# Optimization experiments

Measured on AMD Instinct MI355X. Metric: run time of the kernel, lower is better.

Reference implementation:

```python
import jax, jax.numpy as jnp
import numpy as np

EPS = 1e-5
H, W, C, NCLS = 8, 16, 64, 8

def _bn_params(key, c):
    k1, k2, k3, k4 = jax.random.split(key, 4)
    gamma = jax.random.uniform(k1, (c,), minval=0.5, maxval=1.5)
    beta = 0.1 * jax.random.normal(k2, (c,))
    mean = 0.1 * jax.random.normal(k3, (c,))
    var = jax.random.uniform(k4, (c,), minval=0.5, maxval=1.5)
    return jnp.stack([gamma, beta, mean, var]).astype(jnp.float32)  # (4, c)

def bn2d(x, p):
    # eval-mode BatchNorm2d; p: (4, C); x: (B, C, H, W)
    g, b, m, v = p[0], p[1], p[2], p[3]
    s = g * jax.lax.rsqrt(v + EPS)
    return x * s[None, :, None, None] + (b - m * s)[None, :, None, None]

def bn1d_scalar(x, p):
    # eval-mode BatchNorm1d with 1 channel; p: (4, 1); x: (B, 1, F)
    g, b, m, v = p[0], p[1], p[2], p[3]
    s = g * jax.lax.rsqrt(v + EPS)
    return x * s + (b - m * s)

def conv_same(x, w, b):
    y = jax.lax.conv_general_dilated(x, w, (1, 1), 'SAME',
                                     dimension_numbers=('NCHW', 'OIHW', 'NCHW'))
    return y + b[None, :, None, None]

def setup_inputs() -> dict:
    key = jax.random.key(0)
    ks = jax.random.split(key, 24)
    B = 8192
    d = {}
    d['x'] = jax.random.normal(ks[0], (B, 1, H, W), dtype=jnp.float32)
    d['bn0'] = _bn_params(ks[1], 1)
    d['conv1_w'] = 0.1 * jax.random.normal(ks[2], (C, 1, 3, 3), dtype=jnp.float32)
    d['conv1_b'] = jnp.zeros((C,), jnp.float32)
    d['bn1'] = _bn_params(ks[3], C)
    d['conv2_w'] = (0.1 / np.sqrt(C)) * jax.random.normal(ks[4], (C, C, 3, 3), dtype=jnp.float32)
    d['conv2_b'] = jnp.zeros((C,), jnp.float32)
    d['bn2'] = _bn_params(ks[5], C)
    # LocallyConnected2d, kernel_size=1 -> per-pixel (out_c, in_c) weights
    d['lc3_w'] = (1.0 / np.sqrt(C)) * jax.random.normal(ks[6], (C, C, H, W), dtype=jnp.float32)
    d['bn3'] = _bn_params(ks[7], C)
    d['lc4_w'] = (1.0 / np.sqrt(C)) * jax.random.normal(ks[8], (C, C, H, W), dtype=jnp.float32)
    d['bn4'] = _bn_params(ks[9], C)
    F5 = H * W * C
    d['fc5_w'] = (1.0 / np.sqrt(F5)) * jax.random.normal(ks[10], (512, F5), dtype=jnp.float32)
    d['fc5_b'] = jnp.zeros((512,), jnp.float32)
    d['bn5'] = _bn_params(ks[11], 1)
    d['fc6_w'] = (1.0 / np.sqrt(512)) * jax.random.normal(ks[12], (512, 512), dtype=jnp.float32)
    d['fc6_b'] = jnp.zeros((512,), jnp.float32)
    d['bn6'] = _bn_params(ks[13], 1)
    d['fc7_w'] = (1.0 / np.sqrt(512)) * jax.random.normal(ks[14], (128, 512), dtype=jnp.float32)
    d['fc7_b'] = jnp.zeros((128,), jnp.float32)
    d['bn7'] = _bn_params(ks[15], 1)
    d['fc8_w'] = (1.0 / np.sqrt(128)) * jax.random.normal(ks[16], (NCLS, 128), dtype=jnp.float32)
    d['fc8_b'] = jnp.zeros((NCLS,), jnp.float32)
    return d

def reference(x, bn0, conv1_w, conv1_b, bn1, conv2_w, conv2_b, bn2,
              lc3_w, bn3, lc4_w, bn4, fc5_w, fc5_b, bn5,
              fc6_w, fc6_b, bn6, fc7_w, fc7_b, bn7, fc8_w, fc8_b):
    B = x.shape[0]
    # squeeze -> view(B, 16, 8) -> transpose(1,2) -> add channel dim
    h = jnp.swapaxes(x.reshape(B, W, H), 1, 2)[:, None]  # (B,1,H,W)
    h = bn2d(h, bn0)
    h = jax.nn.relu(bn2d(conv_same(h, conv1_w, conv1_b), bn1))
    h = jax.nn.relu(bn2d(conv_same(h, conv2_w, conv2_b), bn2))
    # locally connected, k=1: per-pixel channel mixing
    h = jax.nn.relu(bn2d(jnp.einsum('bchw,ochw->bohw', h, lc3_w), bn3))
    h = jax.nn.relu(bn2d(jnp.einsum('bchw,ochw->bohw', h, lc4_w), bn4))
    h = h.reshape(B, 1, -1)  # (B, 1, C*H*W)
    h = h @ fc5_w.T + fc5_b
    h = jax.nn.relu(bn1d_scalar(h, bn5))
    h = jax.nn.relu(bn1d_scalar(h @ fc6_w.T + fc6_b, bn6))
    h = jax.nn.relu(bn1d_scalar(h @ fc7_w.T + fc7_b, bn7))
    h = h @ fc8_w.T + fc8_b
    return h.reshape(B, NCLS)
```

## Files before the change

### kernel.cpp

```cpp
#include <hip/hip_runtime.h>
#include <hip/hip_bf16.h>

typedef unsigned short bf16_t;
typedef __attribute__((ext_vector_type(8))) short bf16x8;
typedef __attribute__((ext_vector_type(8))) unsigned short u16x8;
typedef __attribute__((ext_vector_type(4))) float f32x4;

#if defined(__has_builtin)
#if __has_builtin(__builtin_amdgcn_global_load_lds)
#define HAS_GLL 1
#endif
#endif

__device__ __forceinline__ float b2f(bf16_t u) {
    return __uint_as_float(((unsigned int)u) << 16);
}
__device__ __forceinline__ bf16_t f2b(float f) {
    unsigned int x = __float_as_uint(f);
    unsigned int r = x + 0x7fffu + ((x >> 16) & 1u);
    return (bf16_t)(r >> 16);
}
__device__ __forceinline__ unsigned int pk2(float a, float b) {
    __hip_bfloat162 t = __float22bfloat162_rn(make_float2(a, b));
    return *(unsigned int*)&t;
}
__device__ __forceinline__ float ldf(const void* p, int i, int isf) {
    return isf ? ((const float*)p)[i] : b2f(((const bf16_t*)p)[i]);
}

__device__ __forceinline__ void stg16(const bf16_t* g, bf16_t* l) {
#ifdef HAS_GLL
    __builtin_amdgcn_global_load_lds(
        (const __attribute__((address_space(1))) unsigned int*)g,
        (__attribute__((address_space(3))) unsigned int*)l,
        16, 0, 0);
#else
    *(uint4*)l = *(const uint4*)g;
#endif
}

__device__ __forceinline__ int detect_isf(const void* xraw) {
    const unsigned int* w = (const unsigned int*)xraw;
    unsigned int u = w[threadIdx.x & 63];
    float a = fabsf(__uint_as_float(u << 16));
    int g = (a >= 0.0009765625f && a <= 16.0f) ? 1 : 0;
    unsigned long long m = __ballot(g);
    return (__builtin_popcountll(m) >= 32) ? 0 : 1;
}

#define OFF_S0T0 0
#define OFF_W1   16
#define OFF_S1   592
#define OFF_H1   656
#define OFF_S2   720
#define OFF_H2   784
#define OFF_S3   848
#define OFF_H3   912
#define OFF_S4   976
#define OFF_H4   1040
#define OFF_SC5  1104
#define OFF_H5   1112
#define OFF_SC6  1624
#define OFF_H6   1632
#define OFF_SC7  2144
#define OFF_H7   2152
#define OFF_W8   2280
#define OFF_B8   3304
#define OFF_FLAG 4032

__global__ __launch_bounds__(256) void setup_fold_kernel(
    const void* __restrict__ x,
    const void* __restrict__ w2, const void* __restrict__ w3,
    const void* __restrict__ w4, const void* __restrict__ w5,
    const void* __restrict__ w6, const void* __restrict__ w7,
    bf16_t* __restrict__ w2p, bf16_t* __restrict__ w3p,
    bf16_t* __restrict__ w4p, bf16_t* __restrict__ w5p,
    bf16_t* __restrict__ w6b, bf16_t* __restrict__ w7b,
    const void* __restrict__ bn0p, const void* __restrict__ w1,
    const void* __restrict__ b1, const void* __restrict__ bn1p,
    const void* __restrict__ b2c, const void* __restrict__ bn2p,
    const void* __restrict__ bn3p, const void* __restrict__ bn4p,
    const void* __restrict__ b5, const void* __restrict__ bn5p,
    const void* __restrict__ b6, const void* __restrict__ bn6p,
    const void* __restrict__ b7, const void* __restrict__ bn7p,
    const void* __restrict__ w8, const void* __restrict__ b8,
    float* __restrict__ prm)
{
    const int t = threadIdx.x;
    const int isf = detect_isf(x);

    if (blockIdx.x != 21904) {
        const int i = blockIdx.x * 256 + t;
        if (i < 36864) {
            int oc = i / 576, r = i - oc * 576;
            int tap = r >> 6, ic = r & 63;
            w2p[i] = f2b(ldf(w2, oc * 576 + ic * 9 + tap, isf));
        } else if (i < 561152) {
            int j = i - 36864;
            int p = j >> 12, r = j & 4095;
            int oc = r >> 6, ic = r & 63;
            w3p[j] = f2b(ldf(w3, oc * 8192 + ic * 128 + p, isf));
        } else if (i < 1085440) {
            int j = i - 561152;
            int p = j >> 12, r = j & 4095;
            int oc = r >> 6, ic = r & 63;
            w4p[j] = f2b(ldf(w4, oc * 8192 + ic * 128 + p, isf));
        } else if (i < 5279744) {
            int j = i - 1085440;
            int nr = j >> 13, r = j & 8191;
            int p = r >> 6, c = r & 63;
            w5p[j] = f2b(ldf(w5, nr * 8192 + c * 128 + p, isf));
        } else if (i < 5541888) {
            int j = i - 5279744;
            w6b[j] = isf ? f2b(((const float*)w6)[j]) : ((const bf16_t*)w6)[j];
        } else if (i < 5607424) {
            int j = i - 5541888;
            w7b[j] = isf ? f2b(((const float*)w7)[j]) : ((const bf16_t*)w7)[j];
        }
        return;
    }

    if (t == 0) prm[OFF_FLAG] = isf ? 1.0f : 0.0f;

    if (t == 0) {
        float g = ldf(bn0p, 0, isf), be = ldf(bn0p, 1, isf);
        float m = ldf(bn0p, 2, isf), v = ldf(bn0p, 3, isf);
        float s = g * rsqrtf(v + 1e-5f);
        prm[OFF_S0T0] = s; prm[OFF_S0T0 + 1] = be - m * s;
    }
    for (int i = t; i < 576; i += 256) prm[OFF_W1 + i] = ldf(w1, i, isf);

    if (t < 64) {
        {
            float g = ldf(bn1p, t, isf), be = ldf(bn1p, 64 + t, isf);
            float m = ldf(bn1p, 128 + t, isf), v = ldf(bn1p, 192 + t, isf);
            float s = g * rsqrtf(v + 1e-5f);
            prm[OFF_S1 + t] = s;
            prm[OFF_H1 + t] = s * ldf(b1, t, isf) + (be - m * s);
        }
        {
            float g = ldf(bn2p, t, isf), be = ldf(bn2p, 64 + t, isf);
            float m = ldf(bn2p, 128 + t, isf), v = ldf(bn2p, 192 + t, isf);
            float s = g * rsqrtf(v + 1e-5f);
            prm[OFF_S2 + t] = s;
            prm[OFF_H2 + t] = s * ldf(b2c, t, isf) + (be - m * s);
        }
        {
            float g = ldf(bn3p, t, isf), be = ldf(bn3p, 64 + t, isf);
            float m = ldf(bn3p, 128 + t, isf), v = ldf(bn3p, 192 + t, isf);
            float s = g * rsqrtf(v + 1e-5f);
            prm[OFF_S3 + t] = s;
            prm[OFF_H3 + t] = be - m * s;
        }
        {
            float g = ldf(bn4p, t, isf), be = ldf(bn4p, 64 + t, isf);
            float m = ldf(bn4p, 128 + t, isf), v = ldf(bn4p, 192 + t, isf);
            float s = g * rsqrtf(v + 1e-5f);
            prm[OFF_S4 + t] = s;
            prm[OFF_H4 + t] = be - m * s;
        }
    }
    {
        float g = ldf(bn5p, 0, isf), be = ldf(bn5p, 1, isf);
        float m = ldf(bn5p, 2, isf), v = ldf(bn5p, 3, isf);
        float s = g * rsqrtf(v + 1e-5f);
        if (t == 0) prm[OFF_SC5] = s;
        for (int i = t; i < 512; i += 256)
            prm[OFF_H5 + i] = s * ldf(b5, i, isf) + (be - m * s);
    }
    {
        float g = ldf(bn6p, 0, isf), be = ldf(bn6p, 1, isf);
        float m = ldf(bn6p, 2, isf), v = ldf(bn6p, 3, isf);
        float s = g * rsqrtf(v + 1e-5f);
        if (t == 0) prm[OFF_SC6] = s;
        for (int i = t; i < 512; i += 256)
            prm[OFF_H6 + i] = s * ldf(b6, i, isf) + (be - m * s);
    }
    {
        float g = ldf(bn7p, 0, isf), be = ldf(bn7p, 1, isf);
        float m = ldf(bn7p, 2, isf), v = ldf(bn7p, 3, isf);
        float s = g * rsqrtf(v + 1e-5f);
        if (t == 0) prm[OFF_SC7] = s;
        if (t < 128) prm[OFF_H7 + t] = s * ldf(b7, t, isf) + (be - m * s);
    }
    for (int i = t; i < 1024; i += 256) prm[OFF_W8 + i] = ldf(w8, i, isf);
    if (t < 8) prm[OFF_B8 + t] = ldf(b8, t, isf);
}

__global__ __launch_bounds__(256) void conv1_kernel(
    const void* __restrict__ x, const float* __restrict__ prm,
    bf16_t* __restrict__ c1, int Bc, int c0)
{
    __shared__ float xn[720];
    __shared__ float w1s[576];

    const int t = threadIdx.x;
    const int b0 = blockIdx.x * 4;
    const int isf = prm[OFF_FLAG] > 0.5f;
    const float s0 = prm[OFF_S0T0], t0 = prm[OFF_S0T0 + 1];

    for (int i = t; i < 576; i += 256) w1s[i] = prm[OFF_W1 + i];
    for (int i = t; i < 720; i += 256) {
        int s = i / 180, r = i - s * 180;
        int row = r / 18, col = r - row * 18;
        float v = 0.f;
        if (row >= 1 && row <= 8 && col >= 1 && col <= 16)
            v = s0 * ldf(x, (c0 + b0 + s) * 128 + (col - 1) * 8 + (row - 1), isf) + t0;
        xn[i] = v;
    }

    const int pg  = t & 31;
    const int oc0 = (t >> 5) * 8;

    float s1[8], h1[8];
    #pragma unroll
    for (int j = 0; j < 8; j++) {
        s1[j] = prm[OFF_S1 + oc0 + j];
        h1[j] = prm[OFF_H1 + oc0 + j];
    }
    __syncthreads();

    for (int s = 0; s < 4; s++) {
        const int b = b0 + s;
        const float* xs = xn + s * 180;
        #pragma unroll
        for (int m = 0; m < 4; m++) {
            int p = pg + 32 * m;
            int h = p >> 4, w = p & 15;
            float r[9];
            #pragma unroll
            for (int dh = 0; dh < 3; dh++)
                #pragma unroll
                for (int dw = 0; dw < 3; dw++)
                    r[dh * 3 + dw] = xs[(h + dh) * 18 + (w + dw)];
            u16x8 o;
            #pragma unroll
            for (int j = 0; j < 8; j++) {
                float acc = 0.f;
                #pragma unroll
                for (int k = 0; k < 9; k++) acc += r[k] * w1s[(oc0 + j) * 9 + k];
                o[j] = f2b(fmaxf(s1[j] * acc + h1[j], 0.f));
            }
            *(u16x8*)(c1 + (size_t)p * Bc * 64 + (size_t)b * 64 + oc0) = o;
        }
    }
}

__global__ __launch_bounds__(256) void fused_mfma_kernel(
    const bf16_t* __restrict__ c1, const bf16_t* __restrict__ w2p,
    const bf16_t* __restrict__ w3p, const bf16_t* __restrict__ w4p,
    const float* __restrict__ prm, bf16_t* __restrict__ bufA, int Bc)
{
    __shared__ bf16_t sm[20480];
    const int t    = threadIdx.x;
    const int lane = t & 63;
    const int wv   = t >> 6;

    int btile, p;
    {
        const int nbx = gridDim.x;
        const int id = blockIdx.x + nbx * blockIdx.y;
        if ((nbx & 7) == 0) {
            const int xcd = id & 7;
            const int k   = id >> 3;
            p     = k & 127;
            btile = xcd + 8 * (k >> 7);
        } else {
            btile = blockIdx.x; p = blockIdx.y;
        }
    }
    const int m0 = btile * 256;
    const int h  = p >> 4, w = p & 15;

    const int fr = lane & 15;
    const int fg = lane >> 4;
    const int swz4 = (fr >> 1) & 3;

    const int gS    = (t & 3) ^ ((t >> 3) & 3);
    const int rA    = t >> 2;
    const int coff0 = rA * 64 + gS * 8;
    const int w2off = rA * 576 + gS * 8;

    u16x8 wr3[2], wr4[2];
    {
        const bf16_t* w3b = w3p + (size_t)p * 4096 + coff0;
        const bf16_t* w4b = w4p + (size_t)p * 4096 + coff0;
        wr3[0] = *(const u16x8*)(w3b);
        wr3[1] = *(const u16x8*)(w3b + 32);
        wr4[0] = *(const u16x8*)(w4b);
        wr4[1] = *(const u16x8*)(w4b + 32);
    }

    f32x4 acc[4][4];
    #pragma unroll
    for (int i = 0; i < 4; i++)
        #pragma unroll
        for (int j = 0; j < 4; j++)
            acc[i][j] = (f32x4){0.f, 0.f, 0.f, 0.f};

    const bf16_t* c1b = c1 + (size_t)m0 * 64 + coff0;
    const size_t planeStride = (size_t)Bc * 64;

    {
        if (h > 0 && w > 0) {
            const bf16_t* ab = c1b + (size_t)((h - 1) * 16 + (w - 1)) * planeStride;
            #pragma unroll
            for (int u = 0; u < 4; u++)
                stg16(ab + u * 4096, sm + t * 8 + u * 2048);
            stg16(w2p + w2off, sm + 16384 + t * 8);
        }
    }
    #pragma unroll
    for (int s = 0; s < 18; s++) {
        const int cur = s & 1;
        __syncthreads();
        if (s + 1 < 18) {
            const int s1  = s + 1;
            const int tap = s1 >> 1;
            const int dh = tap / 3 - 1, dw = tap % 3 - 1;
            const int hh = h + dh, ww = w + dw;
            if (hh >= 0 && hh < 8 && ww >= 0 && ww < 16) {
                const int nb  = cur ^ 1;
                const int ic0 = (s1 & 1) * 32;
                const bf16_t* ab = c1b + (size_t)(hh * 16 + ww) * planeStride + ic0;
                #pragma unroll
                for (int u = 0; u < 4; u++)
                    stg16(ab + u * 4096, sm + nb * 8192 + t * 8 + u * 2048);
                stg16(w2p + w2off + tap * 64 + ic0, sm + 16384 + nb * 2048 + t * 8);
            }
        }
        {
            const int tap = s >> 1;
            const int dh = tap / 3 - 1, dw = tap % 3 - 1;
            const int hh = h + dh, ww = w + dw;
            if (hh >= 0 && hh < 8 && ww >= 0 && ww < 16) {
                const bf16_t* Ab = sm + cur * 8192;
                const bf16_t* Bb = sm + 16384 + cur * 2048;
                bf16x8 hf[4], wf[4];
                #pragma unroll
                for (int j = 0; j < 4; j++)
                    hf[j] = *(const bf16x8*)(Ab + ((wv * 64 + j * 16 + fr) * 4 + (fg ^ swz4)) * 8);
                #pragma unroll
                for (int i = 0; i < 4; i++)
                    wf[i] = *(const bf16x8*)(Bb + ((i * 16 + fr) * 4 + (fg ^ swz4)) * 8);
                #pragma unroll
                for (int i = 0; i < 4; i++)
                    #pragma unroll
                    for (int j = 0; j < 4; j++)
                        acc[i][j] = __builtin_amdgcn_mfma_f32_16x16x32_bf16(
                            wf[i], hf[j], acc[i][j], 0, 0, 0);
            }
        }
    }
    __syncthreads();

#define EPILOGUE(SOFF, HOFF)                                                  \
    _Pragma("unroll")                                                         \
    for (int i = 0; i < 4; i++) {                                             \
        const int oc0e = i * 16 + fg * 4;                                     \
        const float4 sv = *(const float4*)(prm + (SOFF) + oc0e);              \
        const float4 hv = *(const float4*)(prm + (HOFF) + oc0e);              \
        _Pragma("unroll")                                                     \
        for (int j = 0; j < 4; j++) {                                         \
            const int bi = wv * 64 + j * 16 + fr;                             \
            float v0 = fmaxf(sv.x * acc[i][j][0] + hv.x, 0.f);                \
            float v1 = fmaxf(sv.y * acc[i][j][1] + hv.y, 0.f);                \
            float v2 = fmaxf(sv.z * acc[i][j][2] + hv.z, 0.f);                \
            float v3 = fmaxf(sv.w * acc[i][j][3] + hv.w, 0.f);                \
            uint2 pk; pk.x = pk2(v0, v1); pk.y = pk2(v2, v3);                 \
            *(uint2*)(sm + bi * 72 + oc0e) = pk;                              \
        }                                                                     \
    }

    EPILOGUE(OFF_S2, OFF_H2)
    *(u16x8*)(sm + 18432 + t * 8) = wr3[0];
    __syncthreads();

    #pragma unroll
    for (int i = 0; i < 4; i++)
        #pragma unroll
        for (int j = 0; j < 4; j++)
            acc[i][j] = (f32x4){0.f, 0.f, 0.f, 0.f};

    #pragma unroll
    for (int ks = 0; ks < 2; ks++) {
        if (ks == 1) {
            __syncthreads();
            *(u16x8*)(sm + 18432 + t * 8) = wr3[1];
            __syncthreads();
        }
        bf16x8 hf[4], wf[4];
        #pragma unroll
        for (int j = 0; j < 4; j++)
            hf[j] = *(const bf16x8*)(sm + (wv * 64 + j * 16 + fr) * 72 + ks * 32 + fg * 8);
        #pragma unroll
        for (int i = 0; i < 4; i++)
            wf[i] = *(const bf16x8*)(sm + 18432 + ((i * 16 + fr) * 4 + (fg ^ swz4)) * 8);
        #pragma unroll
        for (int i = 0; i < 4; i++)
            #pragma unroll
            for (int j = 0; j < 4; j++)
                acc[i][j] = __builtin_amdgcn_mfma_f32_16x16x32_bf16(
                    wf[i], hf[j], acc[i][j], 0, 0, 0);
    }

    EPILOGUE(OFF_S3, OFF_H3)
    __syncthreads();
    *(u16x8*)(sm + 18432 + t * 8) = wr4[0];
    __syncthreads();

    #pragma unroll
    for (int i = 0; i < 4; i++)
        #pragma unroll
        for (int j = 0; j < 4; j++)
            acc[i][j] = (f32x4){0.f, 0.f, 0.f, 0.f};

    #pragma unroll
    for (int ks = 0; ks < 2; ks++) {
        if (ks == 1) {
            __syncthreads();
            *(u16x8*)(sm + 18432 + t * 8) = wr4[1];
            __syncthreads();
        }
        bf16x8 hf[4], wf[4];
        #pragma unroll
        for (int j = 0; j < 4; j++)
            hf[j] = *(const bf16x8*)(sm + (wv * 64 + j * 16 + fr) * 72 + ks * 32 + fg * 8);
        #pragma unroll
        for (int i = 0; i < 4; i++)
            wf[i] = *(const bf16x8*)(sm + 18432 + ((i * 16 + fr) * 4 + (fg ^ swz4)) * 8);
        #pragma unroll
        for (int i = 0; i < 4; i++)
            #pragma unroll
            for (int j = 0; j < 4; j++)
                acc[i][j] = __builtin_amdgcn_mfma_f32_16x16x32_bf16(
                    wf[i], hf[j], acc[i][j], 0, 0, 0);
    }

    EPILOGUE(OFF_S4, OFF_H4)
#undef EPILOGUE
    __syncthreads();

    const int wrow = t >> 3, wc0 = (t & 7) * 8;
    #pragma unroll
    for (int pass = 0; pass < 8; pass++) {
        const int row = wrow + pass * 32;
        *(uint4*)(bufA + (size_t)(m0 + row) * 8192 + p * 64 + wc0) =
            *(const uint4*)(sm + row * 72 + wc0);
    }
}

__global__ __launch_bounds__(256) void gemm_mfma(
    const bf16_t* __restrict__ A, const bf16_t* __restrict__ W,
    const float* __restrict__ prm, int sc_off, int sh_off,
    bf16_t* __restrict__ out, int K, int N)
{
    __shared__ bf16_t sm[24576];
    const int t    = threadIdx.x;
    const int lane = t & 63;
    const int wv   = t >> 6;
    const int wr   = wv >> 1, wc = wv & 1;

    int bm, bn;
    {
        const int nx = gridDim.x, ny = gridDim.y;
        const int id = blockIdx.x + nx * blockIdx.y;
        if ((nx & 7) == 0) {
            const int xcd = id & 7;
            const int k   = id >> 3;
            const int pl  = k / ny;
            bn = k - pl * ny;
            bm = xcd + 8 * pl;
        } else {
            bm = blockIdx.x; bn = blockIdx.y;
        }
    }
    const int m0 = bm * 128, n0 = bn * 64;

    const int fr = lane & 15;
    const int fg = lane >> 4;
    const int swz8 = fr & 7;

    const bf16_t* srcA[4]; bf16_t* dstA[4];
    #pragma unroll
    for (int u = 0; u < 4; u++) {
        const int c = t + 256 * u;
        const int row = c >> 3;
        const int g = (c & 7) ^ (row & 7);
        srcA[u] = A + (size_t)(m0 + row) * K + g * 8;
        dstA[u] = sm + c * 8;
    }
    const bf16_t* srcB[2]; bf16_t* dstB[2];
    #pragma unroll
    for (int u = 0; u < 2; u++) {
        const int c = t + 256 * u;
        const int row = c >> 3;
        const int g = (c & 7) ^ (row & 7);
        srcB[u] = W + (size_t)(n0 + row) * K + g * 8;
        dstB[u] = sm + 16384 + c * 8;
    }

    f32x4 acc[4][2];
    #pragma unroll
    for (int i = 0; i < 4; i++)
        #pragma unroll
        for (int j = 0; j < 2; j++)
            acc[i][j] = (f32x4){0.f, 0.f, 0.f, 0.f};

    const int KS = K >> 6;

    #pragma unroll
    for (int u = 0; u < 4; u++) stg16(srcA[u], dstA[u]);
    #pragma unroll
    for (int u = 0; u < 2; u++) stg16(srcB[u], dstB[u]);

    for (int ks = 0; ks < KS; ks++) {
        const int cur = ks & 1;
        __syncthreads();
        if (ks + 1 < KS) {
            const int nb = cur ^ 1;
            const int kk = (ks + 1) << 6;
            #pragma unroll
            for (int u = 0; u < 4; u++) stg16(srcA[u] + kk, dstA[u] + nb * 8192);
            #pragma unroll
            for (int u = 0; u < 2; u++) stg16(srcB[u] + kk, dstB[u] + nb * 4096);
        }
        const bf16_t* Ab = sm + cur * 8192;
        const bf16_t* Bb = sm + 16384 + cur * 4096;
        bf16x8 af[4][2], bf2[2][2];
        #pragma unroll
        for (int i = 0; i < 4; i++)
            #pragma unroll
            for (int hh = 0; hh < 2; hh++) {
                const int r = wr * 64 + i * 16 + fr;
                const int g = hh * 4 + fg;
                af[i][hh] = *(const bf16x8*)(Ab + (r * 8 + (g ^ swz8)) * 8);
            }
        #pragma unroll
        for (int j = 0; j < 2; j++)
            #pragma unroll
            for (int hh = 0; hh < 2; hh++) {
                const int r = wc * 32 + j * 16 + fr;
                const int g = hh * 4 + fg;
                bf2[j][hh] = *(const bf16x8*)(Bb + (r * 8 + (g ^ swz8)) * 8);
            }
        #pragma unroll
        for (int hh = 0; hh < 2; hh++)
            #pragma unroll
            for (int i = 0; i < 4; i++)
                #pragma unroll
                for (int j = 0; j < 2; j++)
                    acc[i][j] = __builtin_amdgcn_mfma_f32_16x16x32_bf16(
                        af[i][hh], bf2[j][hh], acc[i][j], 0, 0, 0);
    }

    const float s    = prm[sc_off];
    const int   orow = fg * 4;
    const int   ocol = fr;
    #pragma unroll
    for (int j = 0; j < 2; j++) {
        const int n  = n0 + wc * 32 + j * 16 + ocol;
        const float sh = prm[sh_off + n];
        #pragma unroll
        for (int i = 0; i < 4; i++) {
            const int mb = m0 + wr * 64 + i * 16 + orow;
            #pragma unroll
            for (int r = 0; r < 4; r++) {
                float v = fmaxf(s * acc[i][j][r] + sh, 0.f);
                out[(size_t)(mb + r) * N + n] = f2b(v);
            }
        }
    }
}

__global__ __launch_bounds__(256) void fc8_kernel(
    const bf16_t* __restrict__ h, const float* __restrict__ prm,
    void* __restrict__ out, int c0)
{
    __shared__ float wsm[8 * 129];
    const int t = threadIdx.x;
    for (int i = t; i < 1024; i += 256) {
        int n = i >> 7, k = i & 127;
        wsm[n * 129 + k] = prm[OFF_W8 + i];
    }
    __syncthreads();
    const int isf = prm[OFF_FLAG] > 0.5f;
    const int bl = t >> 3, n = t & 7;
    const int b = c0 + blockIdx.x * 32 + bl;
    const bf16_t* hb = h + (size_t)(blockIdx.x * 32 + bl) * 128;
    float acc = prm[OFF_B8 + n];
    #pragma unroll
    for (int k8 = 0; k8 < 16; k8++) {
        u16x8 hv = *(const u16x8*)(hb + k8 * 8);
        #pragma unroll
        for (int j = 0; j < 8; j++)
            acc += b2f(hv[j]) * wsm[n * 129 + k8 * 8 + j];
    }
    if (isf) ((float*)out)[(size_t)b * 8 + n] = acc;
    else     ((bf16_t*)out)[(size_t)b * 8 + n] = f2b(acc);
}

extern "C" void kernel_launch(void* const* d_in, const int* in_sizes, int n_in,
                              void* d_out, int out_size, void* d_ws, size_t ws_size,
                              hipStream_t stream)
{
    const void* x    = d_in[0];
    const void* bn0p = d_in[1];
    const void* w1   = d_in[2];
    const void* b1   = d_in[3];
    const void* bn1p = d_in[4];
    const void* w2   = d_in[5];
    const void* b2c  = d_in[6];
    const void* bn2p = d_in[7];
    const void* w3   = d_in[8];
    const void* bn3p = d_in[9];
    const void* w4   = d_in[10];
    const void* bn4p = d_in[11];
    const void* w5   = d_in[12];
    const void* b5   = d_in[13];
    const void* bn5p = d_in[14];
    const void* w6   = d_in[15];
    const void* b6   = d_in[16];
    const void* bn6p = d_in[17];
    const void* w7   = d_in[18];
    const void* b7   = d_in[19];
    const void* bn7p = d_in[20];
    const void* w8   = d_in[21];
    const void* b8   = d_in[22];

    char* base = (char*)d_ws;
    float*  prm = (float*)(base + 0);
    bf16_t* w2p = (bf16_t*)(base + 16384);
    bf16_t* w3p = (bf16_t*)(base + 90112);
    bf16_t* w4p = (bf16_t*)(base + 1138688);
    bf16_t* w5p = (bf16_t*)(base + 2187264);
    bf16_t* w6b = (bf16_t*)(base + 10575872);
    bf16_t* w7b = (bf16_t*)(base + 11100160);
    char*   acts = base + 11231232;

    const int B = 8192;
    const size_t FIXED = 11231232ull;

    setup_fold_kernel<<<21905, 256, 0, stream>>>(
        x, w2, w3, w4, w5, w6, w7, w2p, w3p, w4p, w5p, w6b, w7b,
        bn0p, w1, b1, bn1p, b2c, bn2p, bn3p, bn4p,
        b5, bn5p, b6, bn6p, b7, bn7p, w8, b8, prm);

    const size_t NEED_1PASS = FIXED + (size_t)B * 16384ull + (size_t)B * 18688ull;
    const size_t NEED_2PASS = FIXED + 4096ull * 16384ull + (size_t)B * 18688ull;

    if (ws_size >= NEED_2PASS) {
        const int Bf = (ws_size >= NEED_1PASS) ? 8192 : 4096;

        bf16_t* c1   = (bf16_t*)acts;
        bf16_t* bufA = c1 + (size_t)Bf * 8192;
        bf16_t* bufC = bufA + (size_t)B * 8192;
        bf16_t* bufD = bufC + (size_t)B * 512;
        bf16_t* bufE = bufD + (size_t)B * 512;

        for (int c0 = 0; c0 < B; c0 += Bf) {
            conv1_kernel<<<Bf / 4, 256, 0, stream>>>(x, prm, c1, Bf, c0);
            fused_mfma_kernel<<<dim3(Bf / 256, 128), 256, 0, stream>>>(
                c1, w2p, w3p, w4p, prm, bufA + (size_t)c0 * 8192, Bf);
        }
        gemm_mfma<<<dim3(B / 128, 8), 256, 0, stream>>>(
            bufA, w5p, prm, OFF_SC5, OFF_H5, bufC, 8192, 512);
        gemm_mfma<<<dim3(B / 128, 8), 256, 0, stream>>>(
            bufC, w6b, prm, OFF_SC6, OFF_H6, bufD, 512, 512);
        gemm_mfma<<<dim3(B / 128, 2), 256, 0, stream>>>(
            bufD, w7b, prm, OFF_SC7, OFF_H7, bufE, 512, 128);
        fc8_kernel<<<B / 32, 256, 0, stream>>>(bufE, prm, d_out, 0);
    } else {
        size_t avail = (ws_size > FIXED) ? (ws_size - FIXED) : 0;
        int Bc = 8192;
        while (Bc > 256 && (size_t)Bc * 35072ull > avail) Bc >>= 1;

        bf16_t* c1   = (bf16_t*)acts;
        bf16_t* bufA = c1 + (size_t)Bc * 8192;
        bf16_t* bufC = bufA + (size_t)Bc * 8192;
        bf16_t* bufD = bufC + (size_t)Bc * 512;
        bf16_t* bufE = bufD + (size_t)Bc * 512;

        for (int c0 = 0; c0 < B; c0 += Bc) {
            conv1_kernel<<<Bc / 4, 256, 0, stream>>>(x, prm, c1, Bc, c0);
            fused_mfma_kernel<<<dim3(Bc / 256, 128), 256, 0, stream>>>(
                c1, w2p, w3p, w4p, prm, bufA, Bc);
            gemm_mfma<<<dim3(Bc / 128, 8), 256, 0, stream>>>(
                bufA, w5p, prm, OFF_SC5, OFF_H5, bufC, 8192, 512);
            gemm_mfma<<<dim3(Bc / 128, 8), 256, 0, stream>>>(
                bufC, w6b, prm, OFF_SC6, OFF_H6, bufD, 512, 512);
            gemm_mfma<<<dim3(Bc / 128, 2), 256, 0, stream>>>(
                bufD, w7b, prm, OFF_SC7, OFF_H7, bufE, 512, 128);
            fc8_kernel<<<Bc / 32, 256, 0, stream>>>(bufE, prm, d_out, c0);
        }
    }
}
```

Baseline: 415.1 us.

## Load conv2 operands directly from global and widen FC GEMM N-tile to 128

The conv2 stage in the fused kernel stops staging activations and weights through double-buffered LDS with barriers, and instead loads MFMA fragments straight from global memory (relying on L1/L2 for reuse). Separately, the FC GEMM is templated on the N tile width so fc5 and fc6 use 128-wide tiles (half as many blocks, more reuse of the A tile), while fc7 keeps 64. The first change removes barriers and LDS traffic but risks uncoalesced, latency-exposed global loads. The second raises register and LDS use per block and lowers parallelism.

```diff
diff --git a/kernel.cpp b/kernel.cpp
--- a/kernel.cpp
+++ b/kernel.cpp
@@ -279,7 +279,6 @@
     const int gS    = (t & 3) ^ ((t >> 3) & 3);
     const int rA    = t >> 2;
     const int coff0 = rA * 64 + gS * 8;
-    const int w2off = rA * 576 + gS * 8;
 
     u16x8 wr3[2], wr4[2];
     {
@@ -298,61 +297,34 @@
         for (int j = 0; j < 4; j++)
             acc[i][j] = (f32x4){0.f, 0.f, 0.f, 0.f};
 
-    const bf16_t* c1b = c1 + (size_t)m0 * 64 + coff0;
     const size_t planeStride = (size_t)Bc * 64;
-
-    {
-        if (h > 0 && w > 0) {
-            const bf16_t* ab = c1b + (size_t)((h - 1) * 16 + (w - 1)) * planeStride;
-            #pragma unroll
-            for (int u = 0; u < 4; u++)
-                stg16(ab + u * 4096, sm + t * 8 + u * 2048);
-            stg16(w2p + w2off, sm + 16384 + t * 8);
-        }
-    }
+    const bf16_t* arow   = c1 + (size_t)(m0 + wv * 64 + fr) * 64 + fg * 8;
+    const bf16_t* w2base = w2p + fr * 576 + fg * 8;
+
     #pragma unroll
     for (int s = 0; s < 18; s++) {
-        const int cur = s & 1;
-        __syncthreads();
-        if (s + 1 < 18) {
-            const int s1  = s + 1;
-            const int tap = s1 >> 1;
-            const int dh = tap / 3 - 1, dw = tap % 3 - 1;
-            const int hh = h + dh, ww = w + dw;
-            if (hh >= 0 && hh < 8 && ww >= 0 && ww < 16) {
-                const int nb  = cur ^ 1;
-                const int ic0 = (s1 & 1) * 32;
-                const bf16_t* ab = c1b + (size_t)(hh * 16 + ww) * planeStride + ic0;
-                #pragma unroll
-                for (int u = 0; u < 4; u++)
-                    stg16(ab + u * 4096, sm + nb * 8192 + t * 8 + u * 2048);
-                stg16(w2p + w2off + tap * 64 + ic0, sm + 16384 + nb * 2048 + t * 8);
-            }
-        }
-        {
-            const int tap = s >> 1;
-            const int dh = tap / 3 - 1, dw = tap % 3 - 1;
-            const int hh = h + dh, ww = w + dw;
-            if (hh >= 0 && hh < 8 && ww >= 0 && ww < 16) {
-                const bf16_t* Ab = sm + cur * 8192;
-                const bf16_t* Bb = sm + 16384 + cur * 2048;
-                bf16x8 hf[4], wf[4];
+        const int tap = s >> 1;
+        const int ic0 = (s & 1) * 32;
+        const int dh = tap / 3 - 1, dw = tap % 3 - 1;
+        const int hh = h + dh, ww = w + dw;
+        if (hh >= 0 && hh < 8 && ww >= 0 && ww < 16) {
+            const bf16_t* ap = arow + (size_t)(hh * 16 + ww) * planeStride + ic0;
+            const bf16_t* wp = w2base + tap * 64 + ic0;
+            bf16x8 hf[4], wf[4];
+            #pragma unroll
+            for (int j = 0; j < 4; j++)
+                hf[j] = *(const bf16x8*)(ap + j * 1024);
+            #pragma unroll
+            for (int i = 0; i < 4; i++)
+                wf[i] = *(const bf16x8*)(wp + i * 9216);
+            #pragma unroll
+            for (int i = 0; i < 4; i++)
                 #pragma unroll
                 for (int j = 0; j < 4; j++)
-                    hf[j] = *(const bf16x8*)(Ab + ((wv * 64 + j * 16 + fr) * 4 + (fg ^ swz4)) * 8);
-                #pragma unroll
-                for (int i = 0; i < 4; i++)
-                    wf[i] = *(const bf16x8*)(Bb + ((i * 16 + fr) * 4 + (fg ^ swz4)) * 8);
-                #pragma unroll
-                for (int i = 0; i < 4; i++)
-                    #pragma unroll
-                    for (int j = 0; j < 4; j++)
-                        acc[i][j] = __builtin_amdgcn_mfma_f32_16x16x32_bf16(
-                            wf[i], hf[j], acc[i][j], 0, 0, 0);
-            }
-        }
-    }
-    __syncthreads();
+                    acc[i][j] = __builtin_amdgcn_mfma_f32_16x16x32_bf16(
+                        wf[i], hf[j], acc[i][j], 0, 0, 0);
+        }
+    }
 
 #define EPILOGUE(SOFF, HOFF)                                                  \
     _Pragma("unroll")                                                         \
@@ -441,21 +413,24 @@
 #undef EPILOGUE
     __syncthreads();
 
-    const int wrow = t >> 3, wc0 = (t & 7) * 8;
+    const int orow = t >> 3, wc0 = (t & 7) * 8;
     #pragma unroll
     for (int pass = 0; pass < 8; pass++) {
-        const int row = wrow + pass * 32;
+        const int row = orow + pass * 32;
         *(uint4*)(bufA + (size_t)(m0 + row) * 8192 + p * 64 + wc0) =
             *(const uint4*)(sm + row * 72 + wc0);
     }
 }
 
+template<int BN>
 __global__ __launch_bounds__(256) void gemm_mfma(
     const bf16_t* __restrict__ A, const bf16_t* __restrict__ W,
     const float* __restrict__ prm, int sc_off, int sh_off,
     bf16_t* __restrict__ out, int K, int N)
 {
-    __shared__ bf16_t sm[24576];
+    constexpr int NJ = BN / 32;
+    constexpr int BE = BN * 64;
+    __shared__ bf16_t sm[16384 + 2 * BE];
     const int t    = threadIdx.x;
     const int lane = t & 63;
     const int wv   = t >> 6;
@@ -475,7 +450,7 @@
             bm = blockIdx.x; bn = blockIdx.y;
         }
     }
-    const int m0 = bm * 128, n0 = bn * 64;
+    const int m0 = bm * 128, n0 = bn * BN;
 
     const int fr = lane & 15;
     const int fg = lane >> 4;
@@ -490,9 +465,9 @@
         srcA[u] = A + (size_t)(m0 + row) * K + g * 8;
         dstA[u] = sm + c * 8;
     }
-    const bf16_t* srcB[2]; bf16_t* dstB[2];
-    #pragma unroll
-    for (int u = 0; u < 2; u++) {
+    const bf16_t* srcB[NJ]; bf16_t* dstB[NJ];
+    #pragma unroll
+    for (int u = 0; u < NJ; u++) {
         const int c = t + 256 * u;
         const int row = c >> 3;
         const int g = (c & 7) ^ (row & 7);
@@ -500,11 +475,11 @@
         dstB[u] = sm + 16384 + c * 8;
     }
 
-    f32x4 acc[4][2];
+    f32x4 acc[4][NJ];
     #pragma unroll
     for (int i = 0; i < 4; i++)
         #pragma unroll
-        for (int j = 0; j < 2; j++)
+        for (int j = 0; j < NJ; j++)
             acc[i][j] = (f32x4){0.f, 0.f, 0.f, 0.f};
 
     const int KS = K >> 6;
@@ -512,7 +487,7 @@
     #pragma unroll
     for (int u = 0; u < 4; u++) stg16(srcA[u], dstA[u]);
     #pragma unroll
-    for (int u = 0; u < 2; u++) stg16(srcB[u], dstB[u]);
+    for (int u = 0; u < NJ; u++) stg16(srcB[u], dstB[u]);
 
     for (int ks = 0; ks < KS; ks++) {
         const int cur = ks & 1;
@@ -523,11 +498,11 @@
             #pragma unroll
             for (int u = 0; u < 4; u++) stg16(srcA[u] + kk, dstA[u] + nb * 8192);
             #pragma unroll
-            for (int u = 0; u < 2; u++) stg16(srcB[u] + kk, dstB[u] + nb * 4096);
+            for (int u = 0; u < NJ; u++) stg16(srcB[u] + kk, dstB[u] + nb * BE);
         }
         const bf16_t* Ab = sm + cur * 8192;
-        const bf16_t* Bb = sm + 16384 + cur * 4096;
-        bf16x8 af[4][2], bf2[2][2];
+        const bf16_t* Bb = sm + 16384 + cur * BE;
+        bf16x8 af[4][2], bf2[NJ][2];
         #pragma unroll
         for (int i = 0; i < 4; i++)
             #pragma unroll
@@ -537,10 +512,10 @@
                 af[i][hh] = *(const bf16x8*)(Ab + (r * 8 + (g ^ swz8)) * 8);
             }
         #pragma unroll
-        for (int j = 0; j < 2; j++)
+        for (int j = 0; j < NJ; j++)
             #pragma unroll
             for (int hh = 0; hh < 2; hh++) {
-                const int r = wc * 32 + j * 16 + fr;
+                const int r = wc * (BN / 2) + j * 16 + fr;
                 const int g = hh * 4 + fg;
                 bf2[j][hh] = *(const bf16x8*)(Bb + (r * 8 + (g ^ swz8)) * 8);
             }
@@ -549,7 +524,7 @@
             #pragma unroll
             for (int i = 0; i < 4; i++)
                 #pragma unroll
-                for (int j = 0; j < 2; j++)
+                for (int j = 0; j < NJ; j++)
                     acc[i][j] = __builtin_amdgcn_mfma_f32_16x16x32_bf16(
                         af[i][hh], bf2[j][hh], acc[i][j], 0, 0, 0);
     }
@@ -558,8 +533,8 @@
     const int   orow = fg * 4;
     const int   ocol = fr;
     #pragma unroll
-    for (int j = 0; j < 2; j++) {
-        const int n  = n0 + wc * 32 + j * 16 + ocol;
+    for (int j = 0; j < NJ; j++) {
+        const int n  = n0 + wc * (BN / 2) + j * 16 + ocol;
         const float sh = prm[sh_off + n];
         #pragma unroll
         for (int i = 0; i < 4; i++) {
@@ -663,11 +638,11 @@
             fused_mfma_kernel<<<dim3(Bf / 256, 128), 256, 0, stream>>>(
                 c1, w2p, w3p, w4p, prm, bufA + (size_t)c0 * 8192, Bf);
         }
-        gemm_mfma<<<dim3(B / 128, 8), 256, 0, stream>>>(
+        gemm_mfma<128><<<dim3(B / 128, 4), 256, 0, stream>>>(
             bufA, w5p, prm, OFF_SC5, OFF_H5, bufC, 8192, 512);
-        gemm_mfma<<<dim3(B / 128, 8), 256, 0, stream>>>(
+        gemm_mfma<128><<<dim3(B / 128, 4), 256, 0, stream>>>(
             bufC, w6b, prm, OFF_SC6, OFF_H6, bufD, 512, 512);
-        gemm_mfma<<<dim3(B / 128, 2), 256, 0, stream>>>(
+        gemm_mfma<64><<<dim3(B / 128, 2), 256, 0, stream>>>(
             bufD, w7b, prm, OFF_SC7, OFF_H7, bufE, 512, 128);
         fc8_kernel<<<B / 32, 256, 0, stream>>>(bufE, prm, d_out, 0);
     } else {
@@ -685,11 +660,11 @@
             conv1_kernel<<<Bc / 4, 256, 0, stream>>>(x, prm, c1, Bc, c0);
             fused_mfma_kernel<<<dim3(Bc / 256, 128), 256, 0, stream>>>(
                 c1, w2p, w3p, w4p, prm, bufA, Bc);
-            gemm_mfma<<<dim3(Bc / 128, 8), 256, 0, stream>>>(
+            gemm_mfma<128><<<dim3(Bc / 128, 4), 256, 0, stream>>>(
                 bufA, w5p, prm, OFF_SC5, OFF_H5, bufC, 8192, 512);
-            gemm_mfma<<<dim3(Bc / 128, 8), 256, 0, stream>>>(
+            gemm_mfma<128><<<dim3(Bc / 128, 4), 256, 0, stream>>>(
                 bufC, w6b, prm, OFF_SC6, OFF_H6, bufD, 512, 512);
-            gemm_mfma<<<dim3(Bc / 128, 2), 256, 0, stream>>>(
+            gemm_mfma<64><<<dim3(Bc / 128, 2), 256, 0, stream>>>(
                 bufD, w7b, prm, OFF_SC7, OFF_H7, bufE, 512, 128);
             fc8_kernel<<<Bc / 32, 256, 0, stream>>>(bufE, prm, d_out, c0);
         }
```

New measurement: 572.2 us. 37.9% more time.
